# Kernel tuning notes

Measured on AMD Instinct MI355X. Metric: run time of the kernel, lower is better.

Reference implementation:

```python
import jax, jax.numpy as jnp
import numpy as np

BN_EPS = 1e-5

def _conv(x, w, b=None, pad=0):
    # x: NCHW, w: OIHW
    y = jax.lax.conv_general_dilated(x, w, (1, 1), [(pad, pad), (pad, pad)],
                                     dimension_numbers=('NCHW', 'OIHW', 'NCHW'))
    if b is not None:
        y = y + b[None, :, None, None]
    return y

def setup_inputs() -> dict:
    key = jax.random.key(0)
    ks = jax.random.split(key, 16)
    B, C, H, W = 8, 10, 128, 128
    IN_DIM = 256
    inp = {
        'f_node': jax.random.normal(ks[0], (B, C, H, W), jnp.float32),
        'h_node0': jax.random.normal(ks[1], (B, C, H, W), jnp.float32),
        'h_node1': jax.random.normal(ks[2], (B, C, H, W), jnp.float32),
        'p_nodes': jax.random.normal(ks[3], (6, B, C, H, W), jnp.float32),
        'xf': jax.random.normal(ks[4], (B, IN_DIM, H, W), jnp.float32),
        # Comp_att: 1x1 conv (2*C -> 1) + bias, then sigmoid
        'att_w': jax.random.normal(ks[5], (1, 2 * C, 1, 1), jnp.float32) * 0.1,
        'att_b': jnp.zeros((1,), jnp.float32),
        # Composition: 3x3 conv (2*C -> C), no bias; BatchNorm (eval-mode stats)
        'rel_w': jax.random.normal(ks[6], (C, 2 * C, 3, 3), jnp.float32) * 0.1,
        'bn_gamma': jnp.ones((C,), jnp.float32),
        'bn_beta': jnp.zeros((C,), jnp.float32),
        'bn_mean': jnp.zeros((C,), jnp.float32),
        'bn_var': jnp.ones((C,), jnp.float32),
        # ConvGRU (1x1 kernels): gates conv (2*C -> 2*C), candidate conv (2*C -> C)
        'gates_w': jax.random.normal(ks[7], (2 * C, 2 * C, 1, 1), jnp.float32) * 0.1,
        'gates_b': jnp.zeros((2 * C,), jnp.float32),
        'can_w': jax.random.normal(ks[8], (C, 2 * C, 1, 1), jnp.float32) * 0.1,
        'can_b': jnp.zeros((C,), jnp.float32),
    }
    return inp

def reference(f_node, h_node0, h_node1, p_nodes, xf,
              att_w, att_b, rel_w, bn_gamma, bn_beta, bn_mean, bn_var,
              gates_w, gates_b, can_w, can_b):
    C = f_node.shape[1]
    # --- Comp_att: sigmoid(1x1 conv over concat of children) -> [B,1,H,W]
    comp_att = jax.nn.sigmoid(_conv(jnp.concatenate([h_node0, h_node1], axis=1), att_w, att_b))
    # --- Composition: sum over children of ReLU(BN(conv3x3(cat[parent, child*att])))
    inv_std = bn_gamma / jnp.sqrt(bn_var + BN_EPS)
    def relation(child):
        y = _conv(jnp.concatenate([f_node, child * comp_att], axis=1), rel_w, pad=1)
        y = (y - bn_mean[None, :, None, None]) * inv_std[None, :, None, None] + bn_beta[None, :, None, None]
        return jax.nn.relu(y)
    comp_h = relation(h_node0) + relation(h_node1)
    # --- ConvGRU update (single step, 1x1 convs): input=comp_h, hidden=f_node
    combined = jnp.concatenate([comp_h, f_node], axis=1)
    gates = _conv(combined, gates_w, gates_b)
    reset = jax.nn.sigmoid(gates[:, :C])
    update = jax.nn.sigmoid(gates[:, C:])
    cand = jnp.tanh(_conv(jnp.concatenate([comp_h, reset * f_node], axis=1), can_w, can_b))
    f_node_new = (1.0 - update) * f_node + update * cand
    return (f_node_new, comp_att)
```

## Files before the change

kernel.cpp:

```cpp
#include <hip/hip_runtime.h>

#define B_   8
#define C_   10
#define H_   128
#define W_   128
#define HWSZ (H_ * W_)
#define CHW  (C_ * HWSZ)

#define TS   16
#define HL   18
#define HSZ  (HL * HL)
#define NTHREADS 256

__device__ __forceinline__ float sigm(float x)  { return 1.0f / (1.0f + __expf(-x)); }
__device__ __forceinline__ float tanh_(float x) { return 1.0f - 2.0f / (__expf(2.0f * x) + 1.0f); }

__global__ __launch_bounds__(NTHREADS) void fused_graph_kernel(
    const float* __restrict__ f_g,
    const float* __restrict__ h0_g,
    const float* __restrict__ h1_g,
    const float* __restrict__ attw_g,
    const float* __restrict__ attb_g,
    const float* __restrict__ relw_g,
    const float* __restrict__ gamma_g,
    const float* __restrict__ beta_g,
    const float* __restrict__ mean_g,
    const float* __restrict__ var_g,
    const float* __restrict__ gw_g,
    const float* __restrict__ gb_g,
    const float* __restrict__ cw_g,
    const float* __restrict__ cb_g,
    float* __restrict__ out_f,
    float* __restrict__ out_att)
{
    __shared__ float4 sIn[C_][HSZ];

    const int tid = threadIdx.x;
    const int bx = blockIdx.x, by = blockIdx.y, b = blockIdx.z;

    float aw[20];
    #pragma unroll
    for (int i = 0; i < 20; i++) aw[i] = attw_g[i];
    const float ab = attb_g[0];

    const int gy0 = by * TS - 1, gx0 = bx * TS - 1;
    for (int p = tid; p < HSZ; p += NTHREADS) {
        const int hy = p / HL, hx = p - hy * HL;
        const int gy = gy0 + hy, gx = gx0 + hx;
        if (gy >= 0 && gy < H_ && gx >= 0 && gx < W_) {
            const int base = b * CHW + gy * W_ + gx;
            float fv[10], h0v[10], h1v[10];
            float acc = ab;
            #pragma unroll
            for (int ci = 0; ci < 10; ci++) {
                fv[ci]  = f_g [base + ci * HWSZ];
                h0v[ci] = h0_g[base + ci * HWSZ];
                h1v[ci] = h1_g[base + ci * HWSZ];
                acc += aw[ci] * h0v[ci] + aw[10 + ci] * h1v[ci];
            }
            const float att = sigm(acc);
            #pragma unroll
            for (int ci = 0; ci < 10; ci++)
                sIn[ci][p] = make_float4(fv[ci], h0v[ci] * att, h1v[ci] * att, att);
        } else {
            #pragma unroll
            for (int ci = 0; ci < 10; ci++)
                sIn[ci][p] = make_float4(0.f, 0.f, 0.f, 0.f);
        }
    }
    __syncthreads();

    const int ly = tid >> 4, lx = tid & 15;
    const int hc = (ly + 1) * HL + (lx + 1);

    float accf[10], acc0[10], acc1[10];
    #pragma unroll
    for (int c = 0; c < 10; c++) { accf[c] = 0.f; acc0[c] = 0.f; acc1[c] = 0.f; }

    #pragma unroll 1
    for (int tap = 0; tap < 9; tap++) {
        const int hi = hc + (tap / 3 - 1) * HL + (tap - (tap / 3) * 3 - 1);
        const float* __restrict__ wt = relw_g + tap;
        #pragma unroll
        for (int ci = 0; ci < 10; ci++) {
            const float4 v = sIn[ci][hi];
            #pragma unroll
            for (int c = 0; c < 10; c++) {
                accf[c] += wt[(c * 20 + ci)      * 9] * v.x;
                const float wa = wt[(c * 20 + 10 + ci) * 9];
                acc0[c] += wa * v.y;
                acc1[c] += wa * v.z;
            }
        }
    }

    float ch[10], fc[10], attv;
    {
        const float4 cv = sIn[0][hc];
        fc[0] = cv.x; attv = cv.w;
    }
    #pragma unroll
    for (int c = 1; c < 10; c++) fc[c] = sIn[c][hc].x;
    #pragma unroll
    for (int c = 0; c < 10; c++) {
        const float sc = gamma_g[c] * rsqrtf(var_g[c] + 1e-5f);
        const float bi = beta_g[c] - mean_g[c] * sc;
        ch[c] = fmaxf((accf[c] + acc0[c]) * sc + bi, 0.f)
              + fmaxf((accf[c] + acc1[c]) * sc + bi, 0.f);
    }

    float g[20];
    #pragma unroll
    for (int o = 0; o < 20; o++) g[o] = gb_g[o];
    #pragma unroll
    for (int i = 0; i < 10; i++) {
        #pragma unroll
        for (int o = 0; o < 20; o++)
            g[o] += ch[i] * gw_g[o * 20 + i] + fc[i] * gw_g[o * 20 + 10 + i];
    }
    float cd[10];
    #pragma unroll
    for (int c = 0; c < 10; c++) cd[c] = cb_g[c];
    #pragma unroll
    for (int i = 0; i < 10; i++) {
        const float rf = sigm(g[i]) * fc[i];
        #pragma unroll
        for (int c = 0; c < 10; c++)
            cd[c] += ch[i] * cw_g[c * 20 + i] + rf * cw_g[c * 20 + 10 + i];
    }

    const int gy = by * TS + ly, gx = bx * TS + lx;
    #pragma unroll
    for (int c = 0; c < 10; c++) {
        const float u = sigm(g[10 + c]);
        out_f[((b * C_ + c) * H_ + gy) * W_ + gx] = (1.f - u) * fc[c] + u * tanh_(cd[c]);
    }
    out_att[(b * H_ + gy) * W_ + gx] = attv;
}

extern "C" void kernel_launch(void* const* d_in, const int* in_sizes, int n_in,
                              void* d_out, int out_size, void* d_ws, size_t ws_size,
                              hipStream_t stream) {
    (void)in_sizes; (void)n_in; (void)d_ws; (void)ws_size; (void)out_size;
    const float* f   = (const float*)d_in[0];
    const float* h0  = (const float*)d_in[1];
    const float* h1  = (const float*)d_in[2];
    const float* aw  = (const float*)d_in[5];
    const float* ab  = (const float*)d_in[6];
    const float* rw  = (const float*)d_in[7];
    const float* gam = (const float*)d_in[8];
    const float* bet = (const float*)d_in[9];
    const float* mea = (const float*)d_in[10];
    const float* var = (const float*)d_in[11];
    const float* gw  = (const float*)d_in[12];
    const float* gb  = (const float*)d_in[13];
    const float* cw  = (const float*)d_in[14];
    const float* cb  = (const float*)d_in[15];

    float* out_f   = (float*)d_out;
    float* out_att = out_f + (B_ * C_ * H_ * W_);

    dim3 grid(W_ / TS, H_ / TS, B_);
    fused_graph_kernel<<<grid, dim3(NTHREADS), 0, stream>>>(
        f, h0, h1, aw, ab, rw, gam, bet, mea, var, gw, gb, cw, cb, out_f, out_att);
}
```

Baseline: 257.3 us.

## Stage BN-folded weights in LDS and compute two pixels per thread

Before the halo load, each block copies the 3x3 conv, gate and candidate weights into shared memory, transposed and padded so they can be read as float4, and folds the BN scale into the conv weights. Threads drop from 256 to 128 and each computes two horizontally adjacent pixels. Each weight read is then reused across two pixels and outputs are written as float2. The intent is to replace strided global/scalar weight loads with vectorised LDS broadcasts and halve weight traffic per pixel. The cost is higher register pressure and fewer threads per block, which may lower occupancy, plus a per-block weight preprocessing pass.

Result: slower. 263.5 us (+2.4%).

```diff
diff --git a/kernel.cpp b/kernel.cpp
--- a/kernel.cpp
+++ b/kernel.cpp
@@ -10,12 +10,15 @@
 #define TS   16
 #define HL   18
 #define HSZ  (HL * HL)
-#define NTHREADS 256
+#define NT   128
 
 __device__ __forceinline__ float sigm(float x)  { return 1.0f / (1.0f + __expf(-x)); }
 __device__ __forceinline__ float tanh_(float x) { return 1.0f - 2.0f / (__expf(2.0f * x) + 1.0f); }
-
-__global__ __launch_bounds__(NTHREADS) void fused_graph_kernel(
+__device__ __forceinline__ float comp(const float4 v, int c) {
+    return c == 0 ? v.x : (c == 1 ? v.y : (c == 2 ? v.z : v.w));
+}
+
+__global__ __launch_bounds__(NT) void fused_graph_kernel(
     const float* __restrict__ f_g,
     const float* __restrict__ h0_g,
     const float* __restrict__ h1_g,
@@ -34,17 +37,50 @@
     float* __restrict__ out_att)
 {
     __shared__ float4 sIn[C_][HSZ];
+    __shared__ float4 sWf[90 * 3];
+    __shared__ float4 sWa[90 * 3];
+    __shared__ float4 sGW[100];
+    __shared__ float4 sCW[60];
+    __shared__ float  sGB[20], sCB[10], sBi[10];
 
     const int tid = threadIdx.x;
     const int bx = blockIdx.x, by = blockIdx.y, b = blockIdx.z;
 
+    float* sWfF = (float*)sWf;
+    float* sWaF = (float*)sWa;
+    for (int i = tid; i < 1800; i += NT) {
+        const int tap = i / 200, r = i - tap * 200, ci = r / 20, j = r - ci * 20;
+        const int c   = (j < 10) ? j : j - 10;
+        const int cin = (j < 10) ? ci : 10 + ci;
+        const float sc = gamma_g[c] * rsqrtf(var_g[c] + 1e-5f);
+        const float v = relw_g[(c * 20 + cin) * 9 + tap] * sc;
+        if (j < 10) sWfF[(tap * 10 + ci) * 12 + c] = v;
+        else        sWaF[(tap * 10 + ci) * 12 + c] = v;
+    }
+    float* sGWF = (float*)sGW;
+    for (int i = tid; i < 400; i += NT) {
+        const int in_c = i / 20, o = i - in_c * 20;
+        sGWF[in_c * 20 + o] = gw_g[o * 20 + in_c];
+    }
+    float* sCWF = (float*)sCW;
+    for (int i = tid; i < 200; i += NT) {
+        const int in_c = i / 10, c = i - in_c * 10;
+        sCWF[in_c * 12 + c] = cw_g[c * 20 + in_c];
+    }
+    if (tid < 20) sGB[tid] = gb_g[tid];
+    if (tid < 10) {
+        sCB[tid] = cb_g[tid];
+        const float sc = gamma_g[tid] * rsqrtf(var_g[tid] + 1e-5f);
+        sBi[tid] = beta_g[tid] - mean_g[tid] * sc;
+    }
+
     float aw[20];
     #pragma unroll
     for (int i = 0; i < 20; i++) aw[i] = attw_g[i];
     const float ab = attb_g[0];
 
     const int gy0 = by * TS - 1, gx0 = bx * TS - 1;
-    for (int p = tid; p < HSZ; p += NTHREADS) {
+    for (int p = tid; p < HSZ; p += NT) {
         const int hy = p / HL, hx = p - hy * HL;
         const int gy = gy0 + hy, gx = gx0 + hx;
         if (gy >= 0 && gy < H_ && gx >= 0 && gx < W_) {
@@ -70,72 +106,107 @@
     }
     __syncthreads();
 
-    const int ly = tid >> 4, lx = tid & 15;
-    const int hc = (ly + 1) * HL + (lx + 1);
-
-    float accf[10], acc0[10], acc1[10];
-    #pragma unroll
-    for (int c = 0; c < 10; c++) { accf[c] = 0.f; acc0[c] = 0.f; acc1[c] = 0.f; }
+    const int ly = tid >> 3, lx = tid & 7;
+    const int hc = (ly + 1) * HL + (2 * lx + 1);
+
+    float accf[2][10], acc0[2][10], acc1[2][10];
+    #pragma unroll
+    for (int c = 0; c < 10; c++) {
+        accf[0][c] = 0.f; accf[1][c] = 0.f;
+        acc0[0][c] = 0.f; acc0[1][c] = 0.f;
+        acc1[0][c] = 0.f; acc1[1][c] = 0.f;
+    }
 
     #pragma unroll 1
     for (int tap = 0; tap < 9; tap++) {
         const int hi = hc + (tap / 3 - 1) * HL + (tap - (tap / 3) * 3 - 1);
-        const float* __restrict__ wt = relw_g + tap;
         #pragma unroll
         for (int ci = 0; ci < 10; ci++) {
-            const float4 v = sIn[ci][hi];
+            const int wb = (tap * 10 + ci) * 3;
+            const float4 wf0 = sWf[wb], wf1 = sWf[wb + 1], wf2 = sWf[wb + 2];
+            const float4 wa0 = sWa[wb], wa1 = sWa[wb + 1], wa2 = sWa[wb + 2];
+            const float4 v0 = sIn[ci][hi];
+            const float4 v1 = sIn[ci][hi + 1];
             #pragma unroll
             for (int c = 0; c < 10; c++) {
-                accf[c] += wt[(c * 20 + ci)      * 9] * v.x;
-                const float wa = wt[(c * 20 + 10 + ci) * 9];
-                acc0[c] += wa * v.y;
-                acc1[c] += wa * v.z;
+                const float4 wfq = (c < 4) ? wf0 : (c < 8 ? wf1 : wf2);
+                const float4 waq = (c < 4) ? wa0 : (c < 8 ? wa1 : wa2);
+                const float wfv = comp(wfq, c & 3);
+                const float wav = comp(waq, c & 3);
+                accf[0][c] += wfv * v0.x; accf[1][c] += wfv * v1.x;
+                acc0[0][c] += wav * v0.y; acc0[1][c] += wav * v1.y;
+                acc1[0][c] += wav * v0.z; acc1[1][c] += wav * v1.z;
             }
         }
     }
 
-    float ch[10], fc[10], attv;
+    float ch[2][10], fc[2][10];
+    float att0, att1;
     {
-        const float4 cv = sIn[0][hc];
-        fc[0] = cv.x; attv = cv.w;
-    }
-    #pragma unroll
-    for (int c = 1; c < 10; c++) fc[c] = sIn[c][hc].x;
+        const float4 c0 = sIn[0][hc], c1 = sIn[0][hc + 1];
+        fc[0][0] = c0.x; fc[1][0] = c1.x; att0 = c0.w; att1 = c1.w;
+    }
+    #pragma unroll
+    for (int c = 1; c < 10; c++) {
+        fc[0][c] = sIn[c][hc].x;
+        fc[1][c] = sIn[c][hc + 1].x;
+    }
     #pragma unroll
     for (int c = 0; c < 10; c++) {
-        const float sc = gamma_g[c] * rsqrtf(var_g[c] + 1e-5f);
-        const float bi = beta_g[c] - mean_g[c] * sc;
-        ch[c] = fmaxf((accf[c] + acc0[c]) * sc + bi, 0.f)
-              + fmaxf((accf[c] + acc1[c]) * sc + bi, 0.f);
-    }
-
-    float g[20];
-    #pragma unroll
-    for (int o = 0; o < 20; o++) g[o] = gb_g[o];
+        const float bi = sBi[c];
+        ch[0][c] = fmaxf(accf[0][c] + acc0[0][c] + bi, 0.f)
+                 + fmaxf(accf[0][c] + acc1[0][c] + bi, 0.f);
+        ch[1][c] = fmaxf(accf[1][c] + acc0[1][c] + bi, 0.f)
+                 + fmaxf(accf[1][c] + acc1[1][c] + bi, 0.f);
+    }
+
+    float g[2][20];
+    #pragma unroll
+    for (int o = 0; o < 20; o++) { g[0][o] = sGB[o]; g[1][o] = sGB[o]; }
     #pragma unroll
     for (int i = 0; i < 10; i++) {
+        const float4 r0a = sGW[i * 5],        r0b = sGW[i * 5 + 1],
+                     r0c = sGW[i * 5 + 2],    r0d = sGW[i * 5 + 3],  r0e = sGW[i * 5 + 4];
+        const float4 r1a = sGW[(10+i) * 5],   r1b = sGW[(10+i) * 5 + 1],
+                     r1c = sGW[(10+i) * 5 + 2], r1d = sGW[(10+i) * 5 + 3], r1e = sGW[(10+i) * 5 + 4];
         #pragma unroll
-        for (int o = 0; o < 20; o++)
-            g[o] += ch[i] * gw_g[o * 20 + i] + fc[i] * gw_g[o * 20 + 10 + i];
-    }
-    float cd[10];
-    #pragma unroll
-    for (int c = 0; c < 10; c++) cd[c] = cb_g[c];
+        for (int o = 0; o < 20; o++) {
+            const float4 w0 = (o < 4) ? r0a : (o < 8 ? r0b : (o < 12 ? r0c : (o < 16 ? r0d : r0e)));
+            const float4 w1 = (o < 4) ? r1a : (o < 8 ? r1b : (o < 12 ? r1c : (o < 16 ? r1d : r1e)));
+            const float wc = comp(w0, o & 3), wfv = comp(w1, o & 3);
+            g[0][o] += ch[0][i] * wc + fc[0][i] * wfv;
+            g[1][o] += ch[1][i] * wc + fc[1][i] * wfv;
+        }
+    }
+    float cd[2][10];
+    #pragma unroll
+    for (int c = 0; c < 10; c++) { cd[0][c] = sCB[c]; cd[1][c] = sCB[c]; }
     #pragma unroll
     for (int i = 0; i < 10; i++) {
-        const float rf = sigm(g[i]) * fc[i];
+        const float4 r0a = sCW[i * 3],      r0b = sCW[i * 3 + 1],      r0c = sCW[i * 3 + 2];
+        const float4 r1a = sCW[(10+i) * 3], r1b = sCW[(10+i) * 3 + 1], r1c = sCW[(10+i) * 3 + 2];
+        const float rf0 = sigm(g[0][i]) * fc[0][i];
+        const float rf1 = sigm(g[1][i]) * fc[1][i];
         #pragma unroll
-        for (int c = 0; c < 10; c++)
-            cd[c] += ch[i] * cw_g[c * 20 + i] + rf * cw_g[c * 20 + 10 + i];
-    }
-
-    const int gy = by * TS + ly, gx = bx * TS + lx;
+        for (int c = 0; c < 10; c++) {
+            const float4 w0 = (c < 4) ? r0a : (c < 8 ? r0b : r0c);
+            const float4 w1 = (c < 4) ? r1a : (c < 8 ? r1b : r1c);
+            const float wc = comp(w0, c & 3), wr = comp(w1, c & 3);
+            cd[0][c] += ch[0][i] * wc + rf0 * wr;
+            cd[1][c] += ch[1][i] * wc + rf1 * wr;
+        }
+    }
+
+    const int gy = by * TS + ly, gx = bx * TS + 2 * lx;
     #pragma unroll
     for (int c = 0; c < 10; c++) {
-        const float u = sigm(g[10 + c]);
-        out_f[((b * C_ + c) * H_ + gy) * W_ + gx] = (1.f - u) * fc[c] + u * tanh_(cd[c]);
-    }
-    out_att[(b * H_ + gy) * W_ + gx] = attv;
+        const float u0 = sigm(g[0][10 + c]);
+        const float u1 = sigm(g[1][10 + c]);
+        float2 v = make_float2((1.f - u0) * fc[0][c] + u0 * tanh_(cd[0][c]),
+                               (1.f - u1) * fc[1][c] + u1 * tanh_(cd[1][c]));
+        *reinterpret_cast<float2*>(&out_f[((b * C_ + c) * H_ + gy) * W_ + gx]) = v;
+    }
+    *reinterpret_cast<float2*>(&out_att[(b * H_ + gy) * W_ + gx]) = make_float2(att0, att1);
 }
 
 extern "C" void kernel_launch(void* const* d_in, const int* in_sizes, int n_in,
@@ -161,6 +232,6 @@
     float* out_att = out_f + (B_ * C_ * H_ * W_);
 
     dim3 grid(W_ / TS, H_ / TS, B_);
-    fused_graph_kernel<<<grid, dim3(NTHREADS), 0, stream>>>(
+    fused_graph_kernel<<<grid, dim3(NT), 0, stream>>>(
         f, h0, h1, aw, ab, rw, gam, bet, mea, var, gw, gb, cw, cb, out_f, out_att);
 }
```
